# Kernel optimization log

Measured on AMD Instinct MI355X. Metric: run time of the kernel, lower is better.

Reference implementation:

```python
import jax, jax.numpy as jnp
import numpy as np

D_MODEL = 1024
N_HEADS = 16
D_HEAD = D_MODEL // N_HEADS
D_FF = 4096
ACT_BITS = 8
GSIZE = 64
EPS = 1e-6


def act_quant(x):
    # per-group int8 activation quantization with straight-through estimator
    qmax = 2.0 ** (ACT_BITS - 1) - 1.0  # 127
    g = x.reshape(x.shape[:-1] + (-1, GSIZE))
    s = jnp.clip(jnp.max(jnp.abs(g), axis=-1, keepdims=True), 1e-5, None) / qmax
    q = jnp.clip(jnp.round(g / s), -qmax, qmax) * s
    out = g + jax.lax.stop_gradient(q - g)  # STE
    return out.reshape(x.shape)


def weight_quant_1b(w):
    # binarize to sign(w) * mean(|w|), STE
    alpha = jnp.mean(jnp.abs(w))
    wq = jnp.sign(w) * alpha
    return w + jax.lax.stop_gradient(wq - w)


def bitlinear(x, w):
    # y = Q_act(x) @ Q_w(w)^T ; w is [out, in]
    return act_quant(x) @ weight_quant_1b(w).T


def rmsnorm(x, g):
    return x * jax.lax.rsqrt(jnp.mean(x * x, axis=-1, keepdims=True) + EPS) * g


def causal_sdpa(q, k, v):
    # q,k,v: [B,H,T,Dh]
    T = q.shape[2]
    scores = jnp.einsum('bhqd,bhkd->bhqk', q, k) / jnp.sqrt(jnp.asarray(D_HEAD, q.dtype))
    mask = jnp.tril(jnp.ones((T, T), dtype=bool))
    scores = jnp.where(mask, scores, jnp.asarray(-1e30, q.dtype))
    p = jax.nn.softmax(scores, axis=-1)
    return jnp.einsum('bhqk,bhkd->bhqd', p, v)


def setup_inputs() -> dict:
    key = jax.random.key(0)
    ks = jax.random.split(key, 11)
    sd = 0.02
    inp = {
        'x': jax.random.normal(ks[0], (1, 4096, D_MODEL), dtype=jnp.float32),
        'wq': jax.random.normal(ks[1], (D_MODEL, D_MODEL), dtype=jnp.float32) * sd,
        'wk': jax.random.normal(ks[2], (D_MODEL, D_MODEL), dtype=jnp.float32) * sd,
        'wv': jax.random.normal(ks[3], (D_MODEL, D_MODEL), dtype=jnp.float32) * sd,
        'wo': jax.random.normal(ks[4], (D_MODEL, D_MODEL), dtype=jnp.float32) * sd,
        'w1': jax.random.normal(ks[5], (D_FF, D_MODEL), dtype=jnp.float32) * sd,
        'w2': jax.random.normal(ks[6], (D_FF, D_MODEL), dtype=jnp.float32) * sd,
        'w3': jax.random.normal(ks[7], (D_MODEL, D_FF), dtype=jnp.float32) * sd,
        'g1': jnp.ones((D_MODEL,), dtype=jnp.float32),
        'g2': jnp.ones((D_MODEL,), dtype=jnp.float32),
    }
    return inp


def reference(x, wq, wk, wv, wo, w1, w2, w3, g1, g2):
    B, T, C = x.shape
    # attention branch
    h = rmsnorm(x, g1)
    q = bitlinear(h, wq).reshape(B, T, N_HEADS, D_HEAD).transpose(0, 2, 1, 3)
    k = bitlinear(h, wk).reshape(B, T, N_HEADS, D_HEAD).transpose(0, 2, 1, 3)
    v = bitlinear(h, wv).reshape(B, T, N_HEADS, D_HEAD).transpose(0, 2, 1, 3)
    y = causal_sdpa(q, k, v).transpose(0, 2, 1, 3).reshape(B, T, C)
    x = x + bitlinear(y, wo)
    # SwiGLU FFN branch
    h2 = rmsnorm(x, g2)
    ff = bitlinear(jax.nn.silu(bitlinear(h2, w1)) * bitlinear(h2, w2), w3)
    return x + ff
```

## Files before the change

kernel.cpp:

```cpp
#include <hip/hip_runtime.h>
#include <math.h>


typedef unsigned short u16;
typedef __attribute__((ext_vector_type(4))) float f32x4;
typedef __attribute__((ext_vector_type(4))) unsigned short u16x4;
typedef __attribute__((ext_vector_type(8))) unsigned short u16x8;
typedef __attribute__((ext_vector_type(8))) __bf16 bf16x8;

#define DEV static __device__ __forceinline__

DEV float bf2f(u16 u) { union { unsigned i; float f; } c; c.i = ((unsigned)u) << 16; return c.f; }
DEV u16 f2bf(float f) { __bf16 b = (__bf16)f; return __builtin_bit_cast(u16, b); }
DEV float fexp2(float x) { float r; asm("v_exp_f32 %0, %1" : "=v"(r) : "v"(x)); return r; }

DEV void gload16(const void* g, void* l) {
  __builtin_amdgcn_global_load_lds((__attribute__((address_space(1))) void*)g,
                                   (__attribute__((address_space(3))) void*)l,
                                   16, 0, 0);
}

__global__ __launch_bounds__(256) void convert_sign_all(
    const float* __restrict__ w0, const float* __restrict__ w1,
    const float* __restrict__ w2, const float* __restrict__ w3,
    const float* __restrict__ w4, const float* __restrict__ w5,
    const float* __restrict__ w6, u16* __restrict__ sgn_base,
    float* __restrict__ partial) {
  __shared__ float red[4];
  const int wi = blockIdx.y;
  const float* srcs[7] = {w0, w1, w2, w3, w4, w5, w6};
  const size_t offs[7] = {0, 1048576, 2097152, 3145728, 4194304, 4194304, 12582912};
  const float* w = srcs[wi];
  u16* sgn = sgn_base + offs[wi];
  const int n4 = (wi < 4) ? 262144 : 1048576;
  const bool ilv = (wi == 4) || (wi == 5);
  const int ilv_add = (wi == 5) ? 64 : 0;

  float s = 0.f;
  for (int i = blockIdx.x * 256 + threadIdx.x; i < n4; i += 256 * 256) {
    f32x4 v = ((const f32x4*)w)[i];
    u16x4 o;
#pragma unroll
    for (int j = 0; j < 4; ++j) {
      float f = v[j];
      o[j] = f > 0.f ? (u16)0x3F80 : (f < 0.f ? (u16)0xBF80 : (u16)0);
      s += fabsf(f);
    }
    size_t di = i;
    if (ilv) {
      int e = i << 2;
      int row = e >> 10, col = e & 1023;
      int dst = ((row >> 6) << 7) + ilv_add + (row & 63);
      di = ((size_t)dst << 8) + (col >> 2);
    }
    ((u16x4*)sgn)[di] = o;
  }
#pragma unroll
  for (int off = 32; off >= 1; off >>= 1) s += __shfl_xor(s, off);
  if ((threadIdx.x & 63) == 0) red[threadIdx.x >> 6] = s;
  __syncthreads();
  if (threadIdx.x == 0)
    partial[wi * 256 + blockIdx.x] = red[0] + red[1] + red[2] + red[3];
}

__global__ __launch_bounds__(256) void finalize_alpha(
    const float* __restrict__ partial, float* __restrict__ alphas) {
  __shared__ float red[4];
  int wi = blockIdx.x;
  float v = partial[wi * 256 + threadIdx.x];
#pragma unroll
  for (int off = 32; off >= 1; off >>= 1) v += __shfl_xor(v, off);
  if ((threadIdx.x & 63) == 0) red[threadIdx.x >> 6] = v;
  __syncthreads();
  if (threadIdx.x == 0)
    alphas[wi] = (red[0] + red[1] + red[2] + red[3]) *
                 (wi < 4 ? (1.f / 1048576.f) : (1.f / 4194304.f));
}

__global__ __launch_bounds__(256) void rmsnorm_quant(
    const float* __restrict__ x, const float* __restrict__ g, u16* __restrict__ out) {
  __shared__ float red[4];
  const int row = blockIdx.x, t = threadIdx.x;
  f32x4 v = ((const f32x4*)(x + (size_t)row * 1024))[t];
  float ss = v[0] * v[0] + v[1] * v[1] + v[2] * v[2] + v[3] * v[3];
#pragma unroll
  for (int off = 32; off >= 1; off >>= 1) ss += __shfl_xor(ss, off);
  if ((t & 63) == 0) red[t >> 6] = ss;
  __syncthreads();
  float tot = red[0] + red[1] + red[2] + red[3];
  float rinv = rsqrtf(tot * (1.f / 1024.f) + 1e-6f);
  f32x4 gg = ((const f32x4*)g)[t];
  float n[4];
#pragma unroll
  for (int j = 0; j < 4; ++j) n[j] = v[j] * rinv * gg[j];
  float gm = fmaxf(fmaxf(fabsf(n[0]), fabsf(n[1])), fmaxf(fabsf(n[2]), fabsf(n[3])));
#pragma unroll
  for (int off = 1; off <= 8; off <<= 1) gm = fmaxf(gm, __shfl_xor(gm, off));
  float s = fmaxf(gm, 1e-5f) / 127.0f;
  u16x4 o;
#pragma unroll
  for (int j = 0; j < 4; ++j) {
    float q = fminf(fmaxf(rintf(n[j] / s), -127.f), 127.f) * s;
    o[j] = f2bf(q);
  }
  ((u16x4*)out)[(size_t)row * 256 + t] = o;
}

__global__ __launch_bounds__(256) void transpose_v(
    const u16* __restrict__ qkv, u16* __restrict__ Vt) {
  __shared__ u16 T[64][65];
  const int tt = blockIdx.x, h = blockIdx.y, tid = threadIdx.x;
#pragma unroll
  for (int i = 0; i < 2; ++i) {
    int idx = i * 2048 + tid * 8;
    int trow = idx >> 6, dcol = idx & 63;
    u16x8 v = *(const u16x8*)(qkv + (size_t)(tt * 64 + trow) * 3072 + 2048 + h * 64 + dcol);
#pragma unroll
    for (int j = 0; j < 8; ++j) T[dcol + j][trow] = v[j];
  }
  __syncthreads();
#pragma unroll
  for (int i = 0; i < 2; ++i) {
    int idx = i * 2048 + tid * 8;
    int drow = idx >> 6, tcol = idx & 63;
    u16x8 v;
#pragma unroll
    for (int j = 0; j < 8; ++j) v[j] = T[drow][tcol + j];
    *(u16x8*)(Vt + ((size_t)h * 64 + drow) * 4096 + tt * 64 + tcol) = v;
  }
}

template <bool RES, int BM>
__global__ __launch_bounds__(256) void gemm_bt(
    const u16* __restrict__ A, const u16* __restrict__ B,
    const float* __restrict__ alpha, int ashift, const float* __restrict__ res,
    void* __restrict__ Cout, int M, int N, int K) {
  constexpr int NI = (BM == 128) ? 4 : 2;
  constexpr int WNE = (BM == 128) ? 64 : 32;
  __shared__ u16 As[BM * 64];
  __shared__ u16 Bs[128 * 64];
  const int tid = threadIdx.x;
  const int l = tid & 63, w = tid >> 6;
  const int wm = (BM == 128) ? (w >> 1) : 0;
  const int wn = (BM == 128) ? (w & 1) : w;
  const int lr = l & 15, lg = l >> 4;
  const int xorv = (l & 7) << 4;
  const int brow = blockIdx.y * BM;
  const int bcol = blockIdx.x * 128;
  const int src_chunk = (l & 7) ^ (l >> 3);
  const int rl = w * 8 + (l >> 3);

  f32x4 acc[4][NI];
#pragma unroll
  for (int i = 0; i < 4; ++i)
#pragma unroll
    for (int j = 0; j < NI; ++j) acc[i][j] = (f32x4){0.f, 0.f, 0.f, 0.f};

  const char* Ag = (const char*)A;
  const char* Bg = (const char*)B;
  const int nkt = K >> 6;
  for (int kt = 0; kt < nkt; ++kt) {
    __syncthreads();
    const size_t kb = (size_t)kt * 128 + src_chunk * 16;
#pragma unroll
    for (int it = 0; it < BM / 32; ++it)
      gload16(Ag + (size_t)(brow + it * 32 + rl) * (size_t)(K * 2) + kb,
              &As[(it * 32 + w * 8) * 64]);
#pragma unroll
    for (int it = 0; it < 4; ++it)
      gload16(Bg + (size_t)(bcol + it * 32 + rl) * (size_t)(K * 2) + kb,
              &Bs[(it * 32 + w * 8) * 64]);
    __syncthreads();

    bf16x8 af[4][2], bfr[NI][2];
#pragma unroll
    for (int mi = 0; mi < 4; ++mi)
#pragma unroll
      for (int ks = 0; ks < 2; ++ks) {
        int row = wm * 64 + mi * 16 + lr;
        af[mi][ks] = *(const bf16x8*)((const char*)As + row * 128 + ((ks * 64 + lg * 16) ^ xorv));
      }
#pragma unroll
    for (int ni = 0; ni < NI; ++ni)
#pragma unroll
      for (int ks = 0; ks < 2; ++ks) {
        int row = wn * WNE + ni * 16 + lr;
        bfr[ni][ks] = *(const bf16x8*)((const char*)Bs + row * 128 + ((ks * 64 + lg * 16) ^ xorv));
      }
#pragma unroll
    for (int ks = 0; ks < 2; ++ks)
#pragma unroll
      for (int mi = 0; mi < 4; ++mi)
#pragma unroll
        for (int ni = 0; ni < NI; ++ni)
          acc[mi][ni] = __builtin_amdgcn_mfma_f32_16x16x32_bf16(
              af[mi][ks], bfr[ni][ks], acc[mi][ni], 0, 0, 0);
  }

  const float scale = alpha[bcol >> ashift];
#pragma unroll
  for (int mi = 0; mi < 4; ++mi)
#pragma unroll
    for (int ni = 0; ni < NI; ++ni)
#pragma unroll
      for (int r = 0; r < 4; ++r) {
        int row = brow + wm * 64 + mi * 16 + lg * 4 + r;
        int col = bcol + wn * WNE + ni * 16 + lr;
        float vv = acc[mi][ni][r] * scale;
        if (RES)
          ((float*)Cout)[(size_t)row * N + col] = res[(size_t)row * N + col] + vv;
        else
          ((u16*)Cout)[(size_t)row * N + col] = f2bf(vv);
      }
}

__global__ __launch_bounds__(256) void gemm_ffn(
    const u16* __restrict__ A, const u16* __restrict__ B12,
    const float* __restrict__ alpha2, u16* __restrict__ zq) {
  __shared__ char smem[32768];
  u16* As = (u16*)smem;
  u16* Bs = (u16*)(smem + 16384);
  float* ex = (float*)smem;

  const int tid = threadIdx.x;
  const int l = tid & 63, w = tid >> 6;
  const int wm = w >> 1, wn = w & 1;
  const int lr = l & 15, lg = l >> 4;
  const int xorv = (l & 7) << 4;
  const int brow = blockIdx.y * 128;
  const int bcol = blockIdx.x * 128;
  const int src_chunk = (l & 7) ^ (l >> 3);
  const int rl = w * 8 + (l >> 3);

  f32x4 acc[4][4];
#pragma unroll
  for (int i = 0; i < 4; ++i)
#pragma unroll
    for (int j = 0; j < 4; ++j) acc[i][j] = (f32x4){0.f, 0.f, 0.f, 0.f};

  for (int kt = 0; kt < 16; ++kt) {
    __syncthreads();
    const size_t kb = (size_t)kt * 128 + src_chunk * 16;
#pragma unroll
    for (int it = 0; it < 4; ++it) {
      gload16((const char*)A + (size_t)(brow + it * 32 + rl) * 2048 + kb,
              &As[(it * 32 + w * 8) * 64]);
      gload16((const char*)B12 + (size_t)(bcol + it * 32 + rl) * 2048 + kb,
              &Bs[(it * 32 + w * 8) * 64]);
    }
    __syncthreads();

    bf16x8 af[4][2], bfr[4][2];
#pragma unroll
    for (int mi = 0; mi < 4; ++mi)
#pragma unroll
      for (int ks = 0; ks < 2; ++ks) {
        int row = wm * 64 + mi * 16 + lr;
        af[mi][ks] = *(const bf16x8*)((const char*)As + row * 128 + ((ks * 64 + lg * 16) ^ xorv));
      }
#pragma unroll
    for (int ni = 0; ni < 4; ++ni)
#pragma unroll
      for (int ks = 0; ks < 2; ++ks) {
        int row = wn * 64 + ni * 16 + lr;
        bfr[ni][ks] = *(const bf16x8*)((const char*)Bs + row * 128 + ((ks * 64 + lg * 16) ^ xorv));
      }
#pragma unroll
    for (int ks = 0; ks < 2; ++ks)
#pragma unroll
      for (int mi = 0; mi < 4; ++mi)
#pragma unroll
        for (int ni = 0; ni < 4; ++ni)
          acc[mi][ni] = __builtin_amdgcn_mfma_f32_16x16x32_bf16(
              af[mi][ks], bfr[ni][ks], acc[mi][ni], 0, 0, 0);
  }

  const float a1 = alpha2[0], a2 = alpha2[1];
  const float L2E = 1.4426950408889634f;
  __syncthreads();
  if (wn == 1) {
#pragma unroll
    for (int mi = 0; mi < 4; ++mi)
#pragma unroll
      for (int ni = 0; ni < 4; ++ni) {
        int col = ni * 16 + lr;
        int row0 = wm * 64 + mi * 16 + lg * 4;
        int rs = row0 ^ ((col & 3) << 3);
        f32x4 t = acc[mi][ni];
        t[0] *= a2; t[1] *= a2; t[2] *= a2; t[3] *= a2;
        *(f32x4*)&ex[col * 128 + rs] = t;
      }
  }
  __syncthreads();
  if (wn == 0) {
#pragma unroll
    for (int mi = 0; mi < 4; ++mi) {
      f32x4 y2v[4];
#pragma unroll
      for (int ni = 0; ni < 4; ++ni) {
        int col = ni * 16 + lr;
        int row0 = wm * 64 + mi * 16 + lg * 4;
        y2v[ni] = *(const f32x4*)&ex[col * 128 + (row0 ^ ((col & 3) << 3))];
      }
#pragma unroll
      for (int r = 0; r < 4; ++r) {
        float zz[4];
        float gm = 0.f;
#pragma unroll
        for (int ni = 0; ni < 4; ++ni) {
          float y1 = acc[mi][ni][r] * a1;
          float sg = y1 / (1.f + fexp2(-L2E * y1));
          zz[ni] = sg * y2v[ni][r];
          gm = fmaxf(gm, fabsf(zz[ni]));
        }
#pragma unroll
        for (int off = 1; off <= 8; off <<= 1) gm = fmaxf(gm, __shfl_xor(gm, off));
        float gmc = fmaxf(gm, 1e-5f);
        float s = gmc * (1.f / 127.f);
        float inv = 127.f / gmc;
        int row = brow + wm * 64 + mi * 16 + lg * 4 + r;
#pragma unroll
        for (int ni = 0; ni < 4; ++ni) {
          int col = blockIdx.x * 64 + ni * 16 + lr;
          float q = fminf(fmaxf(rintf(zz[ni] * inv), -127.f), 127.f) * s;
          zq[(size_t)row * 4096 + col] = f2bf(q);
        }
      }
    }
  }
}

__global__ __launch_bounds__(256) void attn_kernel(
    const u16* __restrict__ QKV, const u16* __restrict__ Vt, u16* __restrict__ Y) {
  __shared__ u16 Ks[2][64 * 64];
  __shared__ u16 Vs[2][64 * 64];
  __shared__ u16 Ps[4][16 * 64];

  const int tid = threadIdx.x;
  const int l = tid & 63, w = tid >> 6;
  const int lr = l & 15, lg = l >> 4;
  const int xorv = (l & 7) << 4;
  const int h = blockIdx.x;
  const int y = blockIdx.y;
  const int qt = (y < 32) ? y : (95 - y);
  const int src_chunk = (l & 7) ^ (l >> 3);
  const int rl = w * 8 + (l >> 3);
  const float SC = 0.18033688f;

  const int qrow0 = qt * 64 + w * 16;
  const int nkt = qt + 1;

  bf16x8 qf[2];
#pragma unroll
  for (int ks = 0; ks < 2; ++ks)
    qf[ks] = __builtin_bit_cast(
        bf16x8, *(const u16x8*)(QKV + (size_t)(qrow0 + lr) * 3072 +
                                h * 64 + ks * 32 + lg * 8));

  f32x4 O[4];
#pragma unroll
  for (int ni = 0; ni < 4; ++ni) O[ni] = (f32x4){0.f, 0.f, 0.f, 0.f};
  float m_ = -3e38f, lsum = 0.f;

  auto STAGE = [&](int buf, int kt) {
#pragma unroll
    for (int it = 0; it < 2; ++it) {
      int krow = kt * 64 + it * 32 + rl;
      gload16((const char*)QKV + ((size_t)krow * 3072 + 1024 + h * 64) * 2 + src_chunk * 16,
              &Ks[buf][(it * 32 + w * 8) * 64]);
      int drow = it * 32 + rl;
      gload16((const char*)Vt + (((size_t)h * 64 + drow) * 4096 + kt * 64) * 2 + src_chunk * 16,
              &Vs[buf][(it * 32 + w * 8) * 64]);
    }
  };

  STAGE(0, 0);
#pragma unroll 1
  for (int kt = 0; kt < nkt; ++kt) {
    const int cur = kt & 1;
    if (kt + 1 < nkt) {
      STAGE(cur ^ 1, kt + 1);
      asm volatile("s_waitcnt vmcnt(4)" ::: "memory");
    } else {
      asm volatile("s_waitcnt vmcnt(0)" ::: "memory");
    }
    __builtin_amdgcn_s_barrier();
    __builtin_amdgcn_sched_barrier(0);

    const char* kbase = (const char*)&Ks[cur][0];
    const char* vbase = (const char*)&Vs[cur][0];

    f32x4 S[4];
    __builtin_amdgcn_s_setprio(1);
#pragma unroll
    for (int ni = 0; ni < 4; ++ni) {
      S[ni] = (f32x4){0.f, 0.f, 0.f, 0.f};
#pragma unroll
      for (int ks = 0; ks < 2; ++ks) {
        bf16x8 kf = *(const bf16x8*)(kbase + (ni * 16 + lr) * 128 +
                                     ((ks * 64 + lg * 16) ^ xorv));
        S[ni] = __builtin_amdgcn_mfma_f32_16x16x32_bf16(kf, qf[ks], S[ni], 0, 0, 0);
      }
    }
    __builtin_amdgcn_s_setprio(0);

#pragma unroll
    for (int ni = 0; ni < 4; ++ni)
#pragma unroll
      for (int r = 0; r < 4; ++r) S[ni][r] *= SC;
    if (kt == qt) {
#pragma unroll
      for (int ni = 0; ni < 4; ++ni)
#pragma unroll
        for (int r = 0; r < 4; ++r)
          if ((ni * 16 + lg * 4 + r) > (w * 16 + lr)) S[ni][r] = -3e38f;
    }

    float nm = -3e38f;
#pragma unroll
    for (int ni = 0; ni < 4; ++ni)
#pragma unroll
      for (int r = 0; r < 4; ++r) nm = fmaxf(nm, S[ni][r]);
    nm = fmaxf(nm, __shfl_xor(nm, 16));
    nm = fmaxf(nm, __shfl_xor(nm, 32));
    if (__ballot(nm > m_ + 8.f)) {
      float mn = fmaxf(m_, nm);
      float fac = fexp2(m_ - mn);
      m_ = mn;
      lsum *= fac;
#pragma unroll
      for (int ni = 0; ni < 4; ++ni) O[ni] *= fac;
    }
    float rs = 0.f;
#pragma unroll
    for (int ni = 0; ni < 4; ++ni)
#pragma unroll
      for (int r = 0; r < 4; ++r) {
        float pv = fexp2(S[ni][r] - m_);
        S[ni][r] = pv;
        rs += pv;
      }
    rs += __shfl_xor(rs, 16);
    rs += __shfl_xor(rs, 32);
    lsum += rs;

#pragma unroll
    for (int ni = 0; ni < 4; ++ni) {
      u16x4 pk;
#pragma unroll
      for (int r = 0; r < 4; ++r) pk[r] = f2bf(S[ni][r]);
      *(u16x4*)((char*)&Ps[w][0] + lr * 128 + ((ni * 32 + lg * 8) ^ xorv)) = pk;
    }
    bf16x8 pt[2];
#pragma unroll
    for (int ks = 0; ks < 2; ++ks)
      pt[ks] = *(const bf16x8*)((const char*)&Ps[w][0] + lr * 128 +
                                ((ks * 64 + lg * 16) ^ xorv));

    __builtin_amdgcn_s_setprio(1);
#pragma unroll
    for (int ni = 0; ni < 4; ++ni) {
#pragma unroll
      for (int ks = 0; ks < 2; ++ks) {
        bf16x8 vf = *(const bf16x8*)(vbase + (ni * 16 + lr) * 128 +
                                     ((ks * 64 + lg * 16) ^ xorv));
        O[ni] = __builtin_amdgcn_mfma_f32_16x16x32_bf16(vf, pt[ks], O[ni], 0, 0, 0);
      }
    }
    __builtin_amdgcn_s_setprio(0);
    asm volatile("" ::: "memory");
    __builtin_amdgcn_s_barrier();
  }

  float rinv = 1.f / lsum;
  float o[4][4];
  float gm = 0.f;
#pragma unroll
  for (int ni = 0; ni < 4; ++ni)
#pragma unroll
    for (int r = 0; r < 4; ++r) {
      o[ni][r] = O[ni][r] * rinv;
      gm = fmaxf(gm, fabsf(o[ni][r]));
    }
  gm = fmaxf(gm, __shfl_xor(gm, 16));
  gm = fmaxf(gm, __shfl_xor(gm, 32));
  float gmc = fmaxf(gm, 1e-5f);
  float s = gmc * (1.f / 127.f);
  float inv = 127.f / gmc;
#pragma unroll
  for (int ni = 0; ni < 4; ++ni) {
    u16x4 ov;
#pragma unroll
    for (int r = 0; r < 4; ++r) {
      float q = fminf(fmaxf(rintf(o[ni][r] * inv), -127.f), 127.f) * s;
      ov[r] = f2bf(q);
    }
    *(u16x4*)(Y + (size_t)(qrow0 + lr) * 1024 + h * 64 + ni * 16 + lg * 4) = ov;
  }
}

extern "C" void kernel_launch(void* const* d_in, const int* in_sizes, int n_in,
                              void* d_out, int out_size, void* d_ws, size_t ws_size,
                              hipStream_t stream) {
  const float* x  = (const float*)d_in[0];
  const float* wq = (const float*)d_in[1];
  const float* wk = (const float*)d_in[2];
  const float* wv = (const float*)d_in[3];
  const float* wo = (const float*)d_in[4];
  const float* w1 = (const float*)d_in[5];
  const float* w2 = (const float*)d_in[6];
  const float* w3 = (const float*)d_in[7];
  const float* g1 = (const float*)d_in[8];
  const float* g2 = (const float*)d_in[9];

  char* ws = (char*)d_ws;
  const size_t MB = 1024 * 1024;
  u16* sgn   = (u16*)ws;
  u16* sWq   = (u16*)(ws + 0 * MB);
  u16* sWo   = (u16*)(ws + 6 * MB);
  u16* sW12  = (u16*)(ws + 8 * MB);
  u16* sW3   = (u16*)(ws + 24 * MB);
  float* partial = (float*)(ws + 32 * MB);
  float* alphas  = (float*)(ws + 32 * MB + 16384);
  u16* Vt    = (u16*)(ws + 33 * MB);
  float* x1  = (float*)(ws + 33 * MB);
  u16* hq    = (u16*)(ws + 49 * MB);
  u16* qkv   = (u16*)(ws + 57 * MB);
  u16* yb    = (u16*)(ws + 81 * MB);
  u16* zq    = (u16*)(ws + 57 * MB);

  convert_sign_all<<<dim3(256, 7), 256, 0, stream>>>(wq, wk, wv, wo, w1, w2, w3,
                                                     sgn, partial);
  finalize_alpha<<<7, 256, 0, stream>>>(partial, alphas);

  rmsnorm_quant<<<4096, 256, 0, stream>>>(x, g1, hq);
  gemm_bt<false, 128><<<dim3(24, 32), 256, 0, stream>>>(hq, sWq, alphas, 10, nullptr,
                                                        qkv, 4096, 3072, 1024);
  transpose_v<<<dim3(64, 16), 256, 0, stream>>>(qkv, Vt);
  attn_kernel<<<dim3(16, 64), 256, 0, stream>>>(qkv, Vt, yb);
  gemm_bt<true, 64><<<dim3(8, 64), 256, 0, stream>>>(yb, sWo, alphas + 3, 31, x,
                                                     x1, 4096, 1024, 1024);
  rmsnorm_quant<<<4096, 256, 0, stream>>>(x1, g2, hq);
  gemm_ffn<<<dim3(64, 32), 256, 0, stream>>>(hq, sW12, alphas + 4, zq);
  gemm_bt<true, 64><<<dim3(8, 64), 256, 0, stream>>>(zq, sW3, alphas + 6, 31, x1,
                                                     (float*)d_out, 4096, 1024, 4096);
}
```

Before: 339.2 us.

## Interleave W1/W2 rows at 16-row granularity so each warp computes silu·gate locally

Changes the interleaved sign-weight layout of W1 and W2 from 64-row to 16-row blocks, so each warp's accumulator tiles hold matching W1 and W2 columns. The FFN GEMM epilogue can then compute silu(y1)*y2 in registers on all warps, with no full-tile exchange through shared memory. Only per-row max values are shared between the warp pair to form the 64-wide quantization group. This removes a large LDS round-trip and the idle half of the warps in the epilogue, and it depends on the layout change and the epilogue indexing agreeing exactly.

```diff
diff --git a/kernel.cpp b/kernel.cpp
--- a/kernel.cpp
+++ b/kernel.cpp
@@ -34,7 +34,7 @@
   u16* sgn = sgn_base + offs[wi];
   const int n4 = (wi < 4) ? 262144 : 1048576;
   const bool ilv = (wi == 4) || (wi == 5);
-  const int ilv_add = (wi == 5) ? 64 : 0;
+  const int ilv_add = (wi == 5) ? 16 : 0;
 
   float s = 0.f;
   for (int i = blockIdx.x * 256 + threadIdx.x; i < n4; i += 256 * 256) {
@@ -50,7 +50,7 @@
     if (ilv) {
       int e = i << 2;
       int row = e >> 10, col = e & 1023;
-      int dst = ((row >> 6) << 7) + ilv_add + (row & 63);
+      int dst = ((row >> 4) << 5) + ilv_add + (row & 15);
       di = ((size_t)dst << 8) + (col >> 2);
     }
     ((u16x4*)sgn)[di] = o;
@@ -217,11 +217,8 @@
 __global__ __launch_bounds__(256) void gemm_ffn(
     const u16* __restrict__ A, const u16* __restrict__ B12,
     const float* __restrict__ alpha2, u16* __restrict__ zq) {
-  __shared__ char smem[32768];
-  u16* As = (u16*)smem;
-  u16* Bs = (u16*)(smem + 16384);
-  float* ex = (float*)smem;
-
+  __shared__ u16 As[128 * 64];
+  __shared__ u16 Bs[128 * 64];
   const int tid = threadIdx.x;
   const int l = tid & 63, w = tid >> 6;
   const int wm = w >> 1, wn = w & 1;
@@ -277,57 +274,47 @@
 
   const float a1 = alpha2[0], a2 = alpha2[1];
   const float L2E = 1.4426950408889634f;
+  float zl[4][4], zh[4][4], rm[4][4];
+#pragma unroll
+  for (int mi = 0; mi < 4; ++mi)
+#pragma unroll
+    for (int r = 0; r < 4; ++r) {
+      float y1 = acc[mi][0][r] * a1;
+      zl[mi][r] = y1 / (1.f + fexp2(-L2E * y1)) * (acc[mi][1][r] * a2);
+      float y3 = acc[mi][2][r] * a1;
+      zh[mi][r] = y3 / (1.f + fexp2(-L2E * y3)) * (acc[mi][3][r] * a2);
+      float g = fmaxf(fabsf(zl[mi][r]), fabsf(zh[mi][r]));
+#pragma unroll
+      for (int off = 1; off <= 8; off <<= 1) g = fmaxf(g, __shfl_xor(g, off));
+      rm[mi][r] = g;
+    }
+
+  float* rmax = (float*)&As[0];
   __syncthreads();
-  if (wn == 1) {
+  if (lr == 0) {
 #pragma unroll
     for (int mi = 0; mi < 4; ++mi)
 #pragma unroll
-      for (int ni = 0; ni < 4; ++ni) {
-        int col = ni * 16 + lr;
-        int row0 = wm * 64 + mi * 16 + lg * 4;
-        int rs = row0 ^ ((col & 3) << 3);
-        f32x4 t = acc[mi][ni];
-        t[0] *= a2; t[1] *= a2; t[2] *= a2; t[3] *= a2;
-        *(f32x4*)&ex[col * 128 + rs] = t;
-      }
+      for (int r = 0; r < 4; ++r)
+        rmax[w * 64 + mi * 16 + lg * 4 + r] = rm[mi][r];
   }
   __syncthreads();
-  if (wn == 0) {
-#pragma unroll
-    for (int mi = 0; mi < 4; ++mi) {
-      f32x4 y2v[4];
-#pragma unroll
-      for (int ni = 0; ni < 4; ++ni) {
-        int col = ni * 16 + lr;
-        int row0 = wm * 64 + mi * 16 + lg * 4;
-        y2v[ni] = *(const f32x4*)&ex[col * 128 + (row0 ^ ((col & 3) << 3))];
-      }
-#pragma unroll
-      for (int r = 0; r < 4; ++r) {
-        float zz[4];
-        float gm = 0.f;
-#pragma unroll
-        for (int ni = 0; ni < 4; ++ni) {
-          float y1 = acc[mi][ni][r] * a1;
-          float sg = y1 / (1.f + fexp2(-L2E * y1));
-          zz[ni] = sg * y2v[ni][r];
-          gm = fmaxf(gm, fabsf(zz[ni]));
-        }
-#pragma unroll
-        for (int off = 1; off <= 8; off <<= 1) gm = fmaxf(gm, __shfl_xor(gm, off));
-        float gmc = fmaxf(gm, 1e-5f);
-        float s = gmc * (1.f / 127.f);
-        float inv = 127.f / gmc;
-        int row = brow + wm * 64 + mi * 16 + lg * 4 + r;
-#pragma unroll
-        for (int ni = 0; ni < 4; ++ni) {
-          int col = blockIdx.x * 64 + ni * 16 + lr;
-          float q = fminf(fmaxf(rintf(zz[ni] * inv), -127.f), 127.f) * s;
-          zq[(size_t)row * 4096 + col] = f2bf(q);
-        }
-      }
-    }
-  }
+
+#pragma unroll
+  for (int mi = 0; mi < 4; ++mi)
+#pragma unroll
+    for (int r = 0; r < 4; ++r) {
+      float g = fmaxf(rm[mi][r], rmax[(w ^ 1) * 64 + mi * 16 + lg * 4 + r]);
+      float gmc = fmaxf(g, 1e-5f);
+      float s = gmc * (1.f / 127.f);
+      float inv = 127.f / gmc;
+      int row = brow + wm * 64 + mi * 16 + lg * 4 + r;
+      int zc = blockIdx.x * 64 + wn * 32 + lr;
+      float q0 = fminf(fmaxf(rintf(zl[mi][r] * inv), -127.f), 127.f) * s;
+      float q1 = fminf(fmaxf(rintf(zh[mi][r] * inv), -127.f), 127.f) * s;
+      zq[(size_t)row * 4096 + zc] = f2bf(q0);
+      zq[(size_t)row * 4096 + zc + 16] = f2bf(q1);
+    }
 }
 
 __global__ __launch_bounds__(256) void attn_kernel(
```

New measurement: 331.8 us. 2.2% less time.
